# Kernel optimization log

Hardware: AMD Instinct MI355X
Metric: run time of the kernel (lower is better)

Reference implementation:

```python
import jax, jax.numpy as jnp
import numpy as np

N = 500_000   # total points
B = 8         # scenes / segments
C = 64        # embedding_dim (= internal_dim, downsample_rate=1)
H = 8         # num_heads


def setup_inputs() -> dict:
    key = jax.random.key(0)
    ks = jax.random.split(key, 12)
    s = 1.0 / np.sqrt(C)
    q = jax.random.normal(ks[0], (N, C), jnp.float32)
    k = jax.random.normal(ks[1], (B, C), jnp.float32)
    v = jax.random.normal(ks[2], (B, C), jnp.float32)
    batch = jnp.sort(jax.random.randint(ks[3], (N,), 0, B)).astype(jnp.int64)
    Wq = jax.random.normal(ks[4], (C, C), jnp.float32) * s
    bq = jnp.zeros((C,), jnp.float32)
    Wk = jax.random.normal(ks[5], (C, C), jnp.float32) * s
    bk = jnp.zeros((C,), jnp.float32)
    Wv = jax.random.normal(ks[6], (C, C), jnp.float32) * s
    bv = jnp.zeros((C,), jnp.float32)
    Wo = jax.random.normal(ks[7], (C, C), jnp.float32) * s
    bo = jnp.zeros((C,), jnp.float32)
    return dict(q=q, k=k, v=v, Wq=Wq, bq=bq, Wk=Wk, bk=bk, Wv=Wv, bv=bv,
                Wo=Wo, bo=bo, batch=batch)


def reference(q, k, v, Wq, bq, Wk, bk, Wv, bv, Wo, bo, batch):
    # Linear projections (nn.Linear applies x @ W.T + b)
    qp = q @ Wq.T + bq            # [N, C]
    kp = k @ Wk.T + bk            # [B, C]
    vp = v @ Wv.T + bv            # [B, C]
    n, c = qp.shape
    d = c // H                    # c_per_head
    nb = kp.shape[0]
    qh = qp.reshape(n, H, d)
    kh = kp.reshape(nb, H, d)[batch]   # gather per point -> [N, H, d]
    vh = vp.reshape(nb, H, d)[batch]   # [N, H, d]
    # elementwise scores, scaled
    attn = qh * kh * (1.0 / np.sqrt(d))  # [N, H, d]
    # segment softmax over the point dim within each batch segment
    m = jax.ops.segment_max(attn, batch, num_segments=nb)   # [B, H, d]
    e = jnp.exp(attn - m[batch])
    z = jax.ops.segment_sum(e, batch, num_segments=nb)      # [B, H, d]
    a = e / z[batch]
    out = (a * vh).reshape(n, c)
    return out @ Wo.T + bo
```

## Files before the change

kernel.cpp:

```cpp
#include <hip/hip_runtime.h>
#include <math.h>

#define NPTS 500000
#define SCALE 0.35355339059327373f
#define NTILES 7813
#define TPB 4
#define GRID ((NTILES + TPB - 1) / TPB)

#define QT_IDX(k, p) ((((k) >> 2) * 276) + (((k) & 3) * 68) + (p))
#define QT_SIZE 4416


__global__ void prep_kernel(const float* __restrict__ kin, const float* __restrict__ vin,
                            const float* __restrict__ Wq, const float* __restrict__ Wk,
                            const float* __restrict__ bk, const float* __restrict__ Wv,
                            const float* __restrict__ bv, const float* __restrict__ Wo,
                            float* __restrict__ ws) {
    const int gid = blockIdx.x * 256 + threadIdx.x;
    float* WqT = ws;
    float* WoT = ws + 4096;
    float* khs = ws + 8192;
    float* vh  = ws + 8704;
    double* zg = (double*)(ws + 9216);
    for (int idx = gid; idx < 4096; idx += 8 * 256) {
        int a = idx >> 6, b = idx & 63;
        WqT[idx] = Wq[b * 64 + a];
        WoT[idx] = Wo[b * 64 + a];
    }
    for (int idx = gid; idx < 512; idx += 8 * 256) {
        int b = idx >> 6, c = idx & 63;
        float dk = 0.f, dv = 0.f;
        #pragma unroll 8
        for (int j = 0; j < 64; ++j) {
            dk = fmaf(kin[b * 64 + j], Wk[c * 64 + j], dk);
            dv = fmaf(vin[b * 64 + j], Wv[c * 64 + j], dv);
        }
        khs[idx] = (dk + bk[c]) * SCALE;
        vh[idx]  = dv + bv[c];
        zg[idx]  = 0.0;
    }
}

__global__ __launch_bounds__(256, 4) void passA_kernel(const float* __restrict__ q,
                                                       const int* __restrict__ batch,
                                                       const float* __restrict__ bq,
                                                       float* __restrict__ ws,
                                                       float* __restrict__ e_out) {
    __shared__ __align__(16) float qT[QT_SIZE];
    __shared__ __align__(16) float wq[4096];
    __shared__ __align__(16) float khs_l[512];
    __shared__ __align__(16) float bq_l[64];
    __shared__ int bs[64];
    __shared__ __align__(16) float zred[4 * 64];

    const float* WqT   = ws;
    const float* khs_g = ws + 8192;
    double* zg = (double*)(ws + 9216);

    const int tid = threadIdx.x;
    const int tx = tid & 15, ty = tid >> 4;

    for (int idx = tid; idx < 1024; idx += 256) ((float4*)wq)[idx] = ((const float4*)WqT)[idx];
    for (int idx = tid; idx < 128; idx += 256) ((float4*)khs_l)[idx] = ((const float4*)khs_g)[idx];
    if (tid < 64) bq_l[tid] = bq[tid];

    float zacc[4] = {0.f, 0.f, 0.f, 0.f};
    int cur_b = -1;

    auto flushz = [&](int b) {
        if (b < 0) return;
        float v0 = zacc[0], v1 = zacc[1], v2 = zacc[2], v3 = zacc[3];
        v0 += __shfl_xor(v0, 16); v0 += __shfl_xor(v0, 32);
        v1 += __shfl_xor(v1, 16); v1 += __shfl_xor(v1, 32);
        v2 += __shfl_xor(v2, 16); v2 += __shfl_xor(v2, 32);
        v3 += __shfl_xor(v3, 16); v3 += __shfl_xor(v3, 32);
        __syncthreads();
        if ((tid & 48) == 0) {
            int wv = tid >> 6;
            *(float4*)&zred[wv * 64 + 4 * tx] = make_float4(v0, v1, v2, v3);
        }
        __syncthreads();
        if (tid < 64) {
            float s = zred[tid] + zred[64 + tid] + zred[128 + tid] + zred[192 + tid];
            unsafeAtomicAdd(&zg[b * 64 + tid], (double)s);
        }
        zacc[0] = zacc[1] = zacc[2] = zacc[3] = 0.f;
    };

    const int t0 = blockIdx.x * TPB;
    const int t1 = (t0 + TPB < NTILES) ? (t0 + TPB) : NTILES;
    __syncthreads();

    float bqa[4];
    { float4 b4 = *(const float4*)&bq_l[4 * tx];
      bqa[0] = b4.x; bqa[1] = b4.y; bqa[2] = b4.z; bqa[3] = b4.w; }

    for (int t = t0; t < t1; ++t) {
        const int p0g = t * 64;
        #pragma unroll
        for (int r = 0; r < 4; ++r) {
            int p = ty + r * 16;
            int gp = p0g + p;
            float4 val = make_float4(0.f, 0.f, 0.f, 0.f);
            if (gp < NPTS) val = ((const float4*)q)[gp * 16 + tx];
            qT[QT_IDX(4 * tx + 0, p)] = val.x;
            qT[QT_IDX(4 * tx + 1, p)] = val.y;
            qT[QT_IDX(4 * tx + 2, p)] = val.z;
            qT[QT_IDX(4 * tx + 3, p)] = val.w;
        }
        if (tid < 64) {
            int gp = p0g + tid;
            bs[tid] = batch[gp < NPTS ? gp : (NPTS - 1)];
        }
        __syncthreads();
        const int b_lo = bs[0], b_hi = bs[63];
        const bool uni = (b_lo == b_hi);
        if (uni) {
            if (cur_b != b_lo) { flushz(cur_b); cur_b = b_lo; }
        } else {
            flushz(cur_b); cur_b = -1;
        }

        float acc[4][4] = {};
        #pragma unroll 4
        for (int kg = 0; kg < 16; ++kg) {
            #pragma unroll
            for (int kj = 0; kj < 4; ++kj) {
                float4 a4 = *(const float4*)&qT[kg * 276 + kj * 68 + 4 * ty];
                float4 w4 = *(const float4*)&wq[(kg * 4 + kj) * 64 + 4 * tx];
                float av[4] = {a4.x, a4.y, a4.z, a4.w};
                float wv[4] = {w4.x, w4.y, w4.z, w4.w};
                #pragma unroll
                for (int i = 0; i < 4; ++i)
                    #pragma unroll
                    for (int j = 0; j < 4; ++j)
                        acc[i][j] = fmaf(av[i], wv[j], acc[i][j]);
            }
        }

        float ev[4][4];
        #pragma unroll
        for (int i = 0; i < 4; ++i) {
            int pl = 4 * ty + i, gp = p0g + pl;
            int bi = bs[pl];
            float4 k4 = *(const float4*)&khs_l[bi * 64 + 4 * tx];
            float kh[4] = {k4.x, k4.y, k4.z, k4.w};
            bool valid = (gp < NPTS);
            #pragma unroll
            for (int j = 0; j < 4; ++j)
                ev[i][j] = valid ? __expf((acc[i][j] + bqa[j]) * kh[j]) : 0.f;
            if (valid)
                ((float4*)e_out)[gp * 16 + tx] = make_float4(ev[i][0], ev[i][1], ev[i][2], ev[i][3]);
        }

        if (uni) {
            #pragma unroll
            for (int j = 0; j < 4; ++j)
                zacc[j] += (ev[0][j] + ev[1][j]) + (ev[2][j] + ev[3][j]);
        } else {
            #pragma unroll
            for (int i = 0; i < 4; ++i) {
                int pl = 4 * ty + i, gp = p0g + pl;
                int bi = bs[pl];
                if (gp < NPTS) {
                    #pragma unroll
                    for (int j = 0; j < 4; ++j)
                        unsafeAtomicAdd(&zg[bi * 64 + 4 * tx + j], (double)ev[i][j]);
                }
            }
        }
        __syncthreads();
    }
    flushz(cur_b);
}

__global__ __launch_bounds__(256, 4) void passB_kernel(const int* __restrict__ batch,
                                                       const float* __restrict__ bo,
                                                       const float* __restrict__ ws,
                                                       float* __restrict__ out) {
    __shared__ __align__(16) float tT[QT_SIZE];
    __shared__ __align__(16) float wo[4096];
    __shared__ __align__(16) float w_l[512];
    __shared__ __align__(16) float bo_l[64];

    const float* WoT  = ws + 4096;
    const float* vh_g = ws + 8704;
    const double* zg  = (const double*)(ws + 9216);

    const int tid = threadIdx.x;
    const int tx = tid & 15, ty = tid >> 4;

    for (int idx = tid; idx < 1024; idx += 256) ((float4*)wo)[idx] = ((const float4*)WoT)[idx];
    for (int idx = tid; idx < 512; idx += 256)
        w_l[idx] = (float)((double)vh_g[idx] / zg[idx]);
    if (tid < 64) bo_l[tid] = bo[tid];

    const int t0 = blockIdx.x * TPB;
    const int t1 = (t0 + TPB < NTILES) ? (t0 + TPB) : NTILES;
    __syncthreads();

    float boa[4];
    { float4 b4 = *(const float4*)&bo_l[4 * tx];
      boa[0] = b4.x; boa[1] = b4.y; boa[2] = b4.z; boa[3] = b4.w; }

    for (int t = t0; t < t1; ++t) {
        const int p0g = t * 64;
        #pragma unroll
        for (int r = 0; r < 4; ++r) {
            int p = ty + r * 16;
            int gp = p0g + p;
            float4 ev = make_float4(0.f, 0.f, 0.f, 0.f);
            int bi = 0;
            if (gp < NPTS) { ev = ((const float4*)out)[gp * 16 + tx]; bi = batch[gp]; }
            float4 wv = *(const float4*)&w_l[bi * 64 + 4 * tx];
            tT[QT_IDX(4 * tx + 0, p)] = ev.x * wv.x;
            tT[QT_IDX(4 * tx + 1, p)] = ev.y * wv.y;
            tT[QT_IDX(4 * tx + 2, p)] = ev.z * wv.z;
            tT[QT_IDX(4 * tx + 3, p)] = ev.w * wv.w;
        }
        __syncthreads();

        float acc[4][4] = {};
        #pragma unroll 4
        for (int cg = 0; cg < 16; ++cg) {
            #pragma unroll
            for (int cj = 0; cj < 4; ++cj) {
                float4 a4 = *(const float4*)&tT[cg * 276 + cj * 68 + 4 * ty];
                float4 w4 = *(const float4*)&wo[(cg * 4 + cj) * 64 + 4 * tx];
                float av[4] = {a4.x, a4.y, a4.z, a4.w};
                float wv[4] = {w4.x, w4.y, w4.z, w4.w};
                #pragma unroll
                for (int i = 0; i < 4; ++i)
                    #pragma unroll
                    for (int j = 0; j < 4; ++j)
                        acc[i][j] = fmaf(av[i], wv[j], acc[i][j]);
            }
        }

        #pragma unroll
        for (int i = 0; i < 4; ++i) {
            int gp = p0g + 4 * ty + i;
            if (gp < NPTS) {
                float4 o = make_float4(acc[i][0] + boa[0], acc[i][1] + boa[1],
                                       acc[i][2] + boa[2], acc[i][3] + boa[3]);
                ((float4*)out)[gp * 16 + tx] = o;
            }
        }
        __syncthreads();
    }
}

extern "C" void kernel_launch(void* const* d_in, const int* in_sizes, int n_in,
                              void* d_out, int out_size, void* d_ws, size_t ws_size,
                              hipStream_t stream) {
    const float* q   = (const float*)d_in[0];
    const float* k   = (const float*)d_in[1];
    const float* v   = (const float*)d_in[2];
    const float* Wq  = (const float*)d_in[3];
    const float* bq  = (const float*)d_in[4];
    const float* Wk  = (const float*)d_in[5];
    const float* bk  = (const float*)d_in[6];
    const float* Wv  = (const float*)d_in[7];
    const float* bv  = (const float*)d_in[8];
    const float* Wo  = (const float*)d_in[9];
    const float* bo  = (const float*)d_in[10];
    const int*  batch = (const int*)d_in[11];
    float* out = (float*)d_out;
    float* ws  = (float*)d_ws;

    prep_kernel<<<8, 256, 0, stream>>>(k, v, Wq, Wk, bk, Wv, bv, Wo, ws);
    passA_kernel<<<GRID, 256, 0, stream>>>(q, batch, bq, ws, out);
    passB_kernel<<<GRID, 256, 0, stream>>>(batch, bo, ws, out);
}
```

Before: 346.2 us.

## Keep weight slices in registers and split K across lanes with LDS reduction

Both GEMM passes now hold a 16x4 slice of the weight matrix in registers per lane, split the 64-wide reduction across four lane groups, and combine partial sums through a padded LDS scratch within each wavefront. The q/out tiles are loaded into LDS with coalesced float4 copies and no transpose, which removes the shared weight copy and the transposed tile. In pass B the per-segment softmax normalizer is folded into the register weights when a tile belongs to a single segment. This trades the LDS weight traffic for more registers per lane and an extra intra-wave reduction step, and relies on wavefront-synchronous LDS access with only a compiler barrier between the write and the read.

```diff
diff --git a/kernel.cpp b/kernel.cpp
--- a/kernel.cpp
+++ b/kernel.cpp
@@ -6,10 +6,18 @@
 #define NTILES 7813
 #define TPB 4
 #define GRID ((NTILES + TPB - 1) / TPB)
-
-#define QT_IDX(k, p) ((((k) >> 2) * 276) + (((k) & 3) * 68) + (p))
-#define QT_SIZE 4416
-
+#define Q4TOT 8000000
+
+
+#define FMA4(A, S, W) do { A.x = fmaf(S, W.x, A.x); A.y = fmaf(S, W.y, A.y); \
+                           A.z = fmaf(S, W.z, A.z); A.w = fmaf(S, W.w, A.w); } while (0)
+
+#define FMABLK(A, a0, a1, a2, a3) do { \
+    FMA4(A, a0.x, wr[0]);  FMA4(A, a0.y, wr[1]);  FMA4(A, a0.z, wr[2]);  FMA4(A, a0.w, wr[3]);  \
+    FMA4(A, a1.x, wr[4]);  FMA4(A, a1.y, wr[5]);  FMA4(A, a1.z, wr[6]);  FMA4(A, a1.w, wr[7]);  \
+    FMA4(A, a2.x, wr[8]);  FMA4(A, a2.y, wr[9]);  FMA4(A, a2.z, wr[10]); FMA4(A, a2.w, wr[11]); \
+    FMA4(A, a3.x, wr[12]); FMA4(A, a3.y, wr[13]); FMA4(A, a3.z, wr[14]); FMA4(A, a3.w, wr[15]); \
+} while (0)
 
 __global__ void prep_kernel(const float* __restrict__ kin, const float* __restrict__ vin,
                             const float* __restrict__ Wq, const float* __restrict__ Wk,
@@ -46,126 +54,127 @@
                                                        const float* __restrict__ bq,
                                                        float* __restrict__ ws,
                                                        float* __restrict__ e_out) {
-    __shared__ __align__(16) float qT[QT_SIZE];
-    __shared__ __align__(16) float wq[4096];
-    __shared__ __align__(16) float khs_l[512];
-    __shared__ __align__(16) float bq_l[64];
-    __shared__ int bs[64];
-    __shared__ __align__(16) float zred[4 * 64];
+    __shared__ __align__(16) float qtile[4096];
+    __shared__ __align__(16) float4 red[4 * 272];
+    __shared__ __align__(16) float zred[256];
 
     const float* WqT   = ws;
     const float* khs_g = ws + 8192;
     double* zg = (double*)(ws + 9216);
 
-    const int tid = threadIdx.x;
-    const int tx = tid & 15, ty = tid >> 4;
-
-    for (int idx = tid; idx < 1024; idx += 256) ((float4*)wq)[idx] = ((const float4*)WqT)[idx];
-    for (int idx = tid; idx < 128; idx += 256) ((float4*)khs_l)[idx] = ((const float4*)khs_g)[idx];
-    if (tid < 64) bq_l[tid] = bq[tid];
-
-    float zacc[4] = {0.f, 0.f, 0.f, 0.f};
+    const int tid  = threadIdx.x;
+    const int wid  = tid >> 6;
+    const int lane = tid & 63;
+    const int tx   = lane & 15;
+    const int ky   = lane >> 4;
+
+    float4* redw = red + wid * 272;
+
+    float4 wr[16];
+    #pragma unroll
+    for (int kk = 0; kk < 16; ++kk)
+        wr[kk] = *(const float4*)&WqT[(ky * 16 + kk) * 64 + 4 * tx];
+
+    const float4 bq4 = ((const float4*)bq)[tx];
+
+    float4 zacc = make_float4(0.f, 0.f, 0.f, 0.f);
     int cur_b = -1;
 
     auto flushz = [&](int b) {
         if (b < 0) return;
-        float v0 = zacc[0], v1 = zacc[1], v2 = zacc[2], v3 = zacc[3];
-        v0 += __shfl_xor(v0, 16); v0 += __shfl_xor(v0, 32);
-        v1 += __shfl_xor(v1, 16); v1 += __shfl_xor(v1, 32);
-        v2 += __shfl_xor(v2, 16); v2 += __shfl_xor(v2, 32);
-        v3 += __shfl_xor(v3, 16); v3 += __shfl_xor(v3, 32);
-        __syncthreads();
-        if ((tid & 48) == 0) {
-            int wv = tid >> 6;
-            *(float4*)&zred[wv * 64 + 4 * tx] = make_float4(v0, v1, v2, v3);
-        }
+        float4 v = zacc;
+        v.x += __shfl_xor(v.x, 16); v.y += __shfl_xor(v.y, 16);
+        v.z += __shfl_xor(v.z, 16); v.w += __shfl_xor(v.w, 16);
+        v.x += __shfl_xor(v.x, 32); v.y += __shfl_xor(v.y, 32);
+        v.z += __shfl_xor(v.z, 32); v.w += __shfl_xor(v.w, 32);
+        __syncthreads();
+        if (ky == 0) *(float4*)&zred[wid * 64 + 4 * tx] = v;
         __syncthreads();
         if (tid < 64) {
             float s = zred[tid] + zred[64 + tid] + zred[128 + tid] + zred[192 + tid];
             unsafeAtomicAdd(&zg[b * 64 + tid], (double)s);
         }
-        zacc[0] = zacc[1] = zacc[2] = zacc[3] = 0.f;
+        zacc = make_float4(0.f, 0.f, 0.f, 0.f);
     };
 
     const int t0 = blockIdx.x * TPB;
     const int t1 = (t0 + TPB < NTILES) ? (t0 + TPB) : NTILES;
-    __syncthreads();
-
-    float bqa[4];
-    { float4 b4 = *(const float4*)&bq_l[4 * tx];
-      bqa[0] = b4.x; bqa[1] = b4.y; bqa[2] = b4.z; bqa[3] = b4.w; }
 
     for (int t = t0; t < t1; ++t) {
         const int p0g = t * 64;
+
         #pragma unroll
-        for (int r = 0; r < 4; ++r) {
-            int p = ty + r * 16;
-            int gp = p0g + p;
-            float4 val = make_float4(0.f, 0.f, 0.f, 0.f);
-            if (gp < NPTS) val = ((const float4*)q)[gp * 16 + tx];
-            qT[QT_IDX(4 * tx + 0, p)] = val.x;
-            qT[QT_IDX(4 * tx + 1, p)] = val.y;
-            qT[QT_IDX(4 * tx + 2, p)] = val.z;
-            qT[QT_IDX(4 * tx + 3, p)] = val.w;
-        }
-        if (tid < 64) {
-            int gp = p0g + tid;
-            bs[tid] = batch[gp < NPTS ? gp : (NPTS - 1)];
-        }
-        __syncthreads();
-        const int b_lo = bs[0], b_hi = bs[63];
+        for (int i = 0; i < 4; ++i) {
+            const int g4 = t * 1024 + i * 256 + tid;
+            float4 v = make_float4(0.f, 0.f, 0.f, 0.f);
+            if (g4 < Q4TOT) v = ((const float4*)q)[g4];
+            ((float4*)qtile)[i * 256 + tid] = v;
+        }
+        const int b_lo = batch[p0g];
+        const int b_hi = batch[(p0g + 63 < NPTS) ? (p0g + 63) : (NPTS - 1)];
         const bool uni = (b_lo == b_hi);
+        __syncthreads();
+
         if (uni) {
             if (cur_b != b_lo) { flushz(cur_b); cur_b = b_lo; }
         } else {
-            flushz(cur_b); cur_b = -1;
-        }
-
-        float acc[4][4] = {};
-        #pragma unroll 4
-        for (int kg = 0; kg < 16; ++kg) {
-            #pragma unroll
-            for (int kj = 0; kj < 4; ++kj) {
-                float4 a4 = *(const float4*)&qT[kg * 276 + kj * 68 + 4 * ty];
-                float4 w4 = *(const float4*)&wq[(kg * 4 + kj) * 64 + 4 * tx];
-                float av[4] = {a4.x, a4.y, a4.z, a4.w};
-                float wv[4] = {w4.x, w4.y, w4.z, w4.w};
-                #pragma unroll
-                for (int i = 0; i < 4; ++i)
-                    #pragma unroll
-                    for (int j = 0; j < 4; ++j)
-                        acc[i][j] = fmaf(av[i], wv[j], acc[i][j]);
-            }
-        }
-
-        float ev[4][4];
-        #pragma unroll
-        for (int i = 0; i < 4; ++i) {
-            int pl = 4 * ty + i, gp = p0g + pl;
-            int bi = bs[pl];
-            float4 k4 = *(const float4*)&khs_l[bi * 64 + 4 * tx];
-            float kh[4] = {k4.x, k4.y, k4.z, k4.w};
-            bool valid = (gp < NPTS);
-            #pragma unroll
-            for (int j = 0; j < 4; ++j)
-                ev[i][j] = valid ? __expf((acc[i][j] + bqa[j]) * kh[j]) : 0.f;
-            if (valid)
-                ((float4*)e_out)[gp * 16 + tx] = make_float4(ev[i][0], ev[i][1], ev[i][2], ev[i][3]);
-        }
-
-        if (uni) {
-            #pragma unroll
-            for (int j = 0; j < 4; ++j)
-                zacc[j] += (ev[0][j] + ev[1][j]) + (ev[2][j] + ev[3][j]);
-        } else {
+            flushz(cur_b);
+            cur_b = -1;
+        }
+
+        const float4 kh4 = *(const float4*)&khs_g[b_lo * 64 + 4 * tx];
+
+        for (int pass = 0; pass < 4; ++pass) {
+            const int pl0 = wid * 16 + pass * 4;
+            float4 acc[4];
+            #pragma unroll
+            for (int i = 0; i < 4; ++i) acc[i] = make_float4(0.f, 0.f, 0.f, 0.f);
+
             #pragma unroll
             for (int i = 0; i < 4; ++i) {
-                int pl = 4 * ty + i, gp = p0g + pl;
-                int bi = bs[pl];
-                if (gp < NPTS) {
-                    #pragma unroll
-                    for (int j = 0; j < 4; ++j)
-                        unsafeAtomicAdd(&zg[bi * 64 + 4 * tx + j], (double)ev[i][j]);
+                const float4* r = (const float4*)(qtile + (pl0 + i) * 64 + ky * 16);
+                const float4 a0 = r[0], a1 = r[1], a2 = r[2], a3 = r[3];
+                FMABLK(acc[i], a0, a1, a2, a3);
+            }
+
+            #pragma unroll
+            for (int i = 0; i < 4; ++i) redw[(i * 4 + ky) * 17 + tx] = acc[i];
+            asm volatile("" ::: "memory");
+            const float4 s0 = redw[(ky * 4 + 0) * 17 + tx];
+            const float4 s1 = redw[(ky * 4 + 1) * 17 + tx];
+            const float4 s2 = redw[(ky * 4 + 2) * 17 + tx];
+            const float4 s3 = redw[(ky * 4 + 3) * 17 + tx];
+            float4 s;
+            s.x = (s0.x + s1.x) + (s2.x + s3.x);
+            s.y = (s0.y + s1.y) + (s2.y + s3.y);
+            s.z = (s0.z + s1.z) + (s2.z + s3.z);
+            s.w = (s0.w + s1.w) + (s2.w + s3.w);
+
+            const int gp = p0g + pl0 + ky;
+            const bool valid = (gp < NPTS);
+
+            if (uni) {
+                float4 e4;
+                e4.x = valid ? __expf((s.x + bq4.x) * kh4.x) : 0.f;
+                e4.y = valid ? __expf((s.y + bq4.y) * kh4.y) : 0.f;
+                e4.z = valid ? __expf((s.z + bq4.z) * kh4.z) : 0.f;
+                e4.w = valid ? __expf((s.w + bq4.w) * kh4.w) : 0.f;
+                if (valid) ((float4*)e_out)[gp * 16 + tx] = e4;
+                zacc.x += e4.x; zacc.y += e4.y; zacc.z += e4.z; zacc.w += e4.w;
+            } else {
+                const int bpt = batch[valid ? gp : (NPTS - 1)];
+                const float4 kh = *(const float4*)&khs_g[bpt * 64 + 4 * tx];
+                float4 e4;
+                e4.x = __expf((s.x + bq4.x) * kh.x);
+                e4.y = __expf((s.y + bq4.y) * kh.y);
+                e4.z = __expf((s.z + bq4.z) * kh.z);
+                e4.w = __expf((s.w + bq4.w) * kh.w);
+                if (valid) {
+                    ((float4*)e_out)[gp * 16 + tx] = e4;
+                    unsafeAtomicAdd(&zg[bpt * 64 + 4 * tx + 0], (double)e4.x);
+                    unsafeAtomicAdd(&zg[bpt * 64 + 4 * tx + 1], (double)e4.y);
+                    unsafeAtomicAdd(&zg[bpt * 64 + 4 * tx + 2], (double)e4.z);
+                    unsafeAtomicAdd(&zg[bpt * 64 + 4 * tx + 3], (double)e4.w);
                 }
             }
         }
@@ -178,71 +187,106 @@
                                                        const float* __restrict__ bo,
                                                        const float* __restrict__ ws,
                                                        float* __restrict__ out) {
-    __shared__ __align__(16) float tT[QT_SIZE];
-    __shared__ __align__(16) float wo[4096];
+    __shared__ __align__(16) float ttile[4096];
+    __shared__ __align__(16) float4 red[4 * 272];
     __shared__ __align__(16) float w_l[512];
-    __shared__ __align__(16) float bo_l[64];
 
     const float* WoT  = ws + 4096;
     const float* vh_g = ws + 8704;
     const double* zg  = (const double*)(ws + 9216);
 
-    const int tid = threadIdx.x;
-    const int tx = tid & 15, ty = tid >> 4;
-
-    for (int idx = tid; idx < 1024; idx += 256) ((float4*)wo)[idx] = ((const float4*)WoT)[idx];
+    const int tid  = threadIdx.x;
+    const int wid  = tid >> 6;
+    const int lane = tid & 63;
+    const int tx   = lane & 15;
+    const int ky   = lane >> 4;
+
+    float4* redw = red + wid * 272;
+
     for (int idx = tid; idx < 512; idx += 256)
         w_l[idx] = (float)((double)vh_g[idx] / zg[idx]);
-    if (tid < 64) bo_l[tid] = bo[tid];
+
+    const float4 bo4 = ((const float4*)bo)[tx];
+
+    float4 wr[16];
+    int wb = -2;
 
     const int t0 = blockIdx.x * TPB;
     const int t1 = (t0 + TPB < NTILES) ? (t0 + TPB) : NTILES;
+
     __syncthreads();
-
-    float boa[4];
-    { float4 b4 = *(const float4*)&bo_l[4 * tx];
-      boa[0] = b4.x; boa[1] = b4.y; boa[2] = b4.z; boa[3] = b4.w; }
 
     for (int t = t0; t < t1; ++t) {
         const int p0g = t * 64;
-        #pragma unroll
-        for (int r = 0; r < 4; ++r) {
-            int p = ty + r * 16;
-            int gp = p0g + p;
-            float4 ev = make_float4(0.f, 0.f, 0.f, 0.f);
-            int bi = 0;
-            if (gp < NPTS) { ev = ((const float4*)out)[gp * 16 + tx]; bi = batch[gp]; }
-            float4 wv = *(const float4*)&w_l[bi * 64 + 4 * tx];
-            tT[QT_IDX(4 * tx + 0, p)] = ev.x * wv.x;
-            tT[QT_IDX(4 * tx + 1, p)] = ev.y * wv.y;
-            tT[QT_IDX(4 * tx + 2, p)] = ev.z * wv.z;
-            tT[QT_IDX(4 * tx + 3, p)] = ev.w * wv.w;
-        }
-        __syncthreads();
-
-        float acc[4][4] = {};
-        #pragma unroll 4
-        for (int cg = 0; cg < 16; ++cg) {
-            #pragma unroll
-            for (int cj = 0; cj < 4; ++cj) {
-                float4 a4 = *(const float4*)&tT[cg * 276 + cj * 68 + 4 * ty];
-                float4 w4 = *(const float4*)&wo[(cg * 4 + cj) * 64 + 4 * tx];
-                float av[4] = {a4.x, a4.y, a4.z, a4.w};
-                float wv[4] = {w4.x, w4.y, w4.z, w4.w};
-                #pragma unroll
-                for (int i = 0; i < 4; ++i)
-                    #pragma unroll
-                    for (int j = 0; j < 4; ++j)
-                        acc[i][j] = fmaf(av[i], wv[j], acc[i][j]);
-            }
-        }
 
         #pragma unroll
         for (int i = 0; i < 4; ++i) {
-            int gp = p0g + 4 * ty + i;
+            const int g4 = t * 1024 + i * 256 + tid;
+            float4 v = make_float4(0.f, 0.f, 0.f, 0.f);
+            if (g4 < Q4TOT) v = ((const float4*)out)[g4];
+            ((float4*)ttile)[i * 256 + tid] = v;
+        }
+        const int b_lo = batch[p0g];
+        const int b_hi = batch[(p0g + 63 < NPTS) ? (p0g + 63) : (NPTS - 1)];
+        const bool uni = (b_lo == b_hi);
+        __syncthreads();
+
+        if (uni) {
+            if (wb != b_lo) {
+                #pragma unroll
+                for (int kk = 0; kk < 16; ++kk) {
+                    const float m = w_l[b_lo * 64 + ky * 16 + kk];
+                    float4 wv = *(const float4*)&WoT[(ky * 16 + kk) * 64 + 4 * tx];
+                    wv.x *= m; wv.y *= m; wv.z *= m; wv.w *= m;
+                    wr[kk] = wv;
+                }
+                wb = b_lo;
+            }
+        } else if (wb != -1) {
+            #pragma unroll
+            for (int kk = 0; kk < 16; ++kk)
+                wr[kk] = *(const float4*)&WoT[(ky * 16 + kk) * 64 + 4 * tx];
+            wb = -1;
+        }
+
+        for (int pass = 0; pass < 4; ++pass) {
+            const int pl0 = wid * 16 + pass * 4;
+            float4 acc[4];
+            #pragma unroll
+            for (int i = 0; i < 4; ++i) acc[i] = make_float4(0.f, 0.f, 0.f, 0.f);
+
+            #pragma unroll
+            for (int i = 0; i < 4; ++i) {
+                const float4* r = (const float4*)(ttile + (pl0 + i) * 64 + ky * 16);
+                float4 a0 = r[0], a1 = r[1], a2 = r[2], a3 = r[3];
+                if (!uni) {
+                    const int gpi = p0g + pl0 + i;
+                    const int bp = batch[(gpi < NPTS) ? gpi : (NPTS - 1)];
+                    const float4* wrow = (const float4*)&w_l[bp * 64 + ky * 16];
+                    const float4 m0 = wrow[0], m1 = wrow[1], m2 = wrow[2], m3 = wrow[3];
+                    a0.x *= m0.x; a0.y *= m0.y; a0.z *= m0.z; a0.w *= m0.w;
+                    a1.x *= m1.x; a1.y *= m1.y; a1.z *= m1.z; a1.w *= m1.w;
+                    a2.x *= m2.x; a2.y *= m2.y; a2.z *= m2.z; a2.w *= m2.w;
+                    a3.x *= m3.x; a3.y *= m3.y; a3.z *= m3.z; a3.w *= m3.w;
+                }
+                FMABLK(acc[i], a0, a1, a2, a3);
+            }
+
+            #pragma unroll
+            for (int i = 0; i < 4; ++i) redw[(i * 4 + ky) * 17 + tx] = acc[i];
+            asm volatile("" ::: "memory");
+            const float4 s0 = redw[(ky * 4 + 0) * 17 + tx];
+            const float4 s1 = redw[(ky * 4 + 1) * 17 + tx];
+            const float4 s2 = redw[(ky * 4 + 2) * 17 + tx];
+            const float4 s3 = redw[(ky * 4 + 3) * 17 + tx];
+
+            const int gp = p0g + pl0 + ky;
             if (gp < NPTS) {
-                float4 o = make_float4(acc[i][0] + boa[0], acc[i][1] + boa[1],
-                                       acc[i][2] + boa[2], acc[i][3] + boa[3]);
+                float4 o;
+                o.x = ((s0.x + s1.x) + (s2.x + s3.x)) + bo4.x;
+                o.y = ((s0.y + s1.y) + (s2.y + s3.y)) + bo4.y;
+                o.z = ((s0.z + s1.z) + (s2.z + s3.z)) + bo4.z;
+                o.w = ((s0.w + s1.w) + (s2.w + s3.w)) + bo4.w;
                 ((float4*)out)[gp * 16 + tx] = o;
             }
         }
```

After: 943.3 us. +172.5%, slower.

## Enlarge point tiles to 128 with 4x8 register blocking in both GEMM passes

Applied to the files above, without the earlier changes.

Both passes now process 128-point tiles with each thread computing a 4x8 output block (two float4 column groups), which roughly halves LDS traffic per FMA. Global loads of q/e are made fully linear float4 reads. The per-tile batch id buffer is replaced by reading the tile's first and last batch ids from global memory, with per-point lookups only on segment-boundary tiles. Bias moves to registers. The cost is more registers and LDS per block, so occupancy drops (launch bounds lowered to 3), and there are fewer tiles per block.

```diff
diff --git a/kernel.cpp b/kernel.cpp
--- a/kernel.cpp
+++ b/kernel.cpp
@@ -3,12 +3,13 @@
 
 #define NPTS 500000
 #define SCALE 0.35355339059327373f
-#define NTILES 7813
-#define TPB 4
-#define GRID ((NTILES + TPB - 1) / TPB)
-
-#define QT_IDX(k, p) ((((k) >> 2) * 276) + (((k) & 3) * 68) + (p))
-#define QT_SIZE 4416
+#define NT128 3907
+#define TPB 2
+#define GRID ((NT128 + TPB - 1) / TPB)
+#define Q4TOT 8000000
+
+#define QTIDX(k, p) ((((k) >> 2) * 532) + (((k) & 3) * 132) + (p))
+#define QT_SZ 8512
 
 
 __global__ void prep_kernel(const float* __restrict__ kin, const float* __restrict__ vin,
@@ -41,131 +42,158 @@
     }
 }
 
-__global__ __launch_bounds__(256, 4) void passA_kernel(const float* __restrict__ q,
+
+__global__ __launch_bounds__(256, 3) void passA_kernel(const float* __restrict__ q,
                                                        const int* __restrict__ batch,
                                                        const float* __restrict__ bq,
                                                        float* __restrict__ ws,
                                                        float* __restrict__ e_out) {
-    __shared__ __align__(16) float qT[QT_SIZE];
+    __shared__ __align__(16) float qT[QT_SZ];
     __shared__ __align__(16) float wq[4096];
     __shared__ __align__(16) float khs_l[512];
-    __shared__ __align__(16) float bq_l[64];
-    __shared__ int bs[64];
-    __shared__ __align__(16) float zred[4 * 64];
+    __shared__ __align__(16) float zred[256];
 
     const float* WqT   = ws;
     const float* khs_g = ws + 8192;
     double* zg = (double*)(ws + 9216);
 
-    const int tid = threadIdx.x;
-    const int tx = tid & 15, ty = tid >> 4;
+    const int tid  = threadIdx.x;
+    const int wid  = tid >> 6;
+    const int lane = tid & 63;
+    const int cc   = tid & 7;
+    const int ty   = tid >> 3;
 
     for (int idx = tid; idx < 1024; idx += 256) ((float4*)wq)[idx] = ((const float4*)WqT)[idx];
     for (int idx = tid; idx < 128; idx += 256) ((float4*)khs_l)[idx] = ((const float4*)khs_g)[idx];
-    if (tid < 64) bq_l[tid] = bq[tid];
-
-    float zacc[4] = {0.f, 0.f, 0.f, 0.f};
+
+    float bqlo[4], bqhi[4];
+    { float4 b4 = ((const float4*)bq)[cc];
+      bqlo[0] = b4.x; bqlo[1] = b4.y; bqlo[2] = b4.z; bqlo[3] = b4.w;
+      b4 = ((const float4*)bq)[8 + cc];
+      bqhi[0] = b4.x; bqhi[1] = b4.y; bqhi[2] = b4.z; bqhi[3] = b4.w; }
+
+    float zacc[8] = {};
     int cur_b = -1;
 
     auto flushz = [&](int b) {
         if (b < 0) return;
-        float v0 = zacc[0], v1 = zacc[1], v2 = zacc[2], v3 = zacc[3];
-        v0 += __shfl_xor(v0, 16); v0 += __shfl_xor(v0, 32);
-        v1 += __shfl_xor(v1, 16); v1 += __shfl_xor(v1, 32);
-        v2 += __shfl_xor(v2, 16); v2 += __shfl_xor(v2, 32);
-        v3 += __shfl_xor(v3, 16); v3 += __shfl_xor(v3, 32);
-        __syncthreads();
-        if ((tid & 48) == 0) {
-            int wv = tid >> 6;
-            *(float4*)&zred[wv * 64 + 4 * tx] = make_float4(v0, v1, v2, v3);
+        #pragma unroll
+        for (int j = 0; j < 8; ++j) {
+            zacc[j] += __shfl_xor(zacc[j], 8);
+            zacc[j] += __shfl_xor(zacc[j], 16);
+            zacc[j] += __shfl_xor(zacc[j], 32);
+        }
+        __syncthreads();
+        if ((lane >> 3) == 0) {
+            *(float4*)&zred[wid * 64 + 4 * cc]      = make_float4(zacc[0], zacc[1], zacc[2], zacc[3]);
+            *(float4*)&zred[wid * 64 + 32 + 4 * cc] = make_float4(zacc[4], zacc[5], zacc[6], zacc[7]);
         }
         __syncthreads();
         if (tid < 64) {
             float s = zred[tid] + zred[64 + tid] + zred[128 + tid] + zred[192 + tid];
             unsafeAtomicAdd(&zg[b * 64 + tid], (double)s);
         }
-        zacc[0] = zacc[1] = zacc[2] = zacc[3] = 0.f;
+        #pragma unroll
+        for (int j = 0; j < 8; ++j) zacc[j] = 0.f;
     };
 
     const int t0 = blockIdx.x * TPB;
-    const int t1 = (t0 + TPB < NTILES) ? (t0 + TPB) : NTILES;
+    const int t1 = (t0 + TPB < NT128) ? (t0 + TPB) : NT128;
     __syncthreads();
 
-    float bqa[4];
-    { float4 b4 = *(const float4*)&bq_l[4 * tx];
-      bqa[0] = b4.x; bqa[1] = b4.y; bqa[2] = b4.z; bqa[3] = b4.w; }
-
     for (int t = t0; t < t1; ++t) {
-        const int p0g = t * 64;
-        #pragma unroll
-        for (int r = 0; r < 4; ++r) {
-            int p = ty + r * 16;
-            int gp = p0g + p;
-            float4 val = make_float4(0.f, 0.f, 0.f, 0.f);
-            if (gp < NPTS) val = ((const float4*)q)[gp * 16 + tx];
-            qT[QT_IDX(4 * tx + 0, p)] = val.x;
-            qT[QT_IDX(4 * tx + 1, p)] = val.y;
-            qT[QT_IDX(4 * tx + 2, p)] = val.z;
-            qT[QT_IDX(4 * tx + 3, p)] = val.w;
-        }
-        if (tid < 64) {
-            int gp = p0g + tid;
-            bs[tid] = batch[gp < NPTS ? gp : (NPTS - 1)];
-        }
-        __syncthreads();
-        const int b_lo = bs[0], b_hi = bs[63];
+        const int p0g = t * 128;
+
+        #pragma unroll
+        for (int i = 0; i < 8; ++i) {
+            const int g4 = t * 2048 + i * 256 + tid;
+            float4 v = make_float4(0.f, 0.f, 0.f, 0.f);
+            if (g4 < Q4TOT) v = ((const float4*)q)[g4];
+            const int pl = i * 16 + (tid >> 4);
+            const int kc = tid & 15;
+            qT[QTIDX(4 * kc + 0, pl)] = v.x;
+            qT[QTIDX(4 * kc + 1, pl)] = v.y;
+            qT[QTIDX(4 * kc + 2, pl)] = v.z;
+            qT[QTIDX(4 * kc + 3, pl)] = v.w;
+        }
+        const int b_lo = batch[p0g];
+        const int b_hi = batch[(p0g + 127 < NPTS) ? (p0g + 127) : (NPTS - 1)];
         const bool uni = (b_lo == b_hi);
+        __syncthreads();
+
         if (uni) {
             if (cur_b != b_lo) { flushz(cur_b); cur_b = b_lo; }
         } else {
-            flushz(cur_b); cur_b = -1;
-        }
-
-        float acc[4][4] = {};
+            flushz(cur_b);
+            cur_b = -1;
+        }
+
+        float acc[4][8] = {};
         #pragma unroll 4
-        for (int kg = 0; kg < 16; ++kg) {
+        for (int kc = 0; kc < 16; ++kc) {
             #pragma unroll
-            for (int kj = 0; kj < 4; ++kj) {
-                float4 a4 = *(const float4*)&qT[kg * 276 + kj * 68 + 4 * ty];
-                float4 w4 = *(const float4*)&wq[(kg * 4 + kj) * 64 + 4 * tx];
-                float av[4] = {a4.x, a4.y, a4.z, a4.w};
-                float wv[4] = {w4.x, w4.y, w4.z, w4.w};
+            for (int j = 0; j < 4; ++j) {
+                const float4 a4  = *(const float4*)&qT[kc * 532 + j * 132 + 4 * ty];
+                const float4 wlo = *(const float4*)&wq[(kc * 4 + j) * 64 + 4 * cc];
+                const float4 whi = *(const float4*)&wq[(kc * 4 + j) * 64 + 32 + 4 * cc];
+                const float av[4] = {a4.x, a4.y, a4.z, a4.w};
+                const float wl[4] = {wlo.x, wlo.y, wlo.z, wlo.w};
+                const float wh[4] = {whi.x, whi.y, whi.z, whi.w};
                 #pragma unroll
-                for (int i = 0; i < 4; ++i)
-                    #pragma unroll
-                    for (int j = 0; j < 4; ++j)
-                        acc[i][j] = fmaf(av[i], wv[j], acc[i][j]);
-            }
-        }
-
-        float ev[4][4];
-        #pragma unroll
-        for (int i = 0; i < 4; ++i) {
-            int pl = 4 * ty + i, gp = p0g + pl;
-            int bi = bs[pl];
-            float4 k4 = *(const float4*)&khs_l[bi * 64 + 4 * tx];
-            float kh[4] = {k4.x, k4.y, k4.z, k4.w};
-            bool valid = (gp < NPTS);
+                for (int i = 0; i < 4; ++i) {
+                    #pragma unroll
+                    for (int m = 0; m < 4; ++m) {
+                        acc[i][m]     = fmaf(av[i], wl[m], acc[i][m]);
+                        acc[i][4 + m] = fmaf(av[i], wh[m], acc[i][4 + m]);
+                    }
+                }
+            }
+        }
+
+        if (uni) {
+            const float4 klo = *(const float4*)&khs_l[b_lo * 64 + 4 * cc];
+            const float4 khi = *(const float4*)&khs_l[b_lo * 64 + 32 + 4 * cc];
+            const float kl[4] = {klo.x, klo.y, klo.z, klo.w};
+            const float kh[4] = {khi.x, khi.y, khi.z, khi.w};
             #pragma unroll
-            for (int j = 0; j < 4; ++j)
-                ev[i][j] = valid ? __expf((acc[i][j] + bqa[j]) * kh[j]) : 0.f;
-            if (valid)
-                ((float4*)e_out)[gp * 16 + tx] = make_float4(ev[i][0], ev[i][1], ev[i][2], ev[i][3]);
-        }
-
-        if (uni) {
-            #pragma unroll
-            for (int j = 0; j < 4; ++j)
-                zacc[j] += (ev[0][j] + ev[1][j]) + (ev[2][j] + ev[3][j]);
+            for (int i = 0; i < 4; ++i) {
+                const int gp = p0g + 4 * ty + i;
+                if (gp < NPTS) {
+                    float e0[4], e1[4];
+                    #pragma unroll
+                    for (int m = 0; m < 4; ++m) {
+                        e0[m] = __expf((acc[i][m] + bqlo[m]) * kl[m]);
+                        e1[m] = __expf((acc[i][4 + m] + bqhi[m]) * kh[m]);
+                    }
+                    ((float4*)e_out)[gp * 16 + cc]     = make_float4(e0[0], e0[1], e0[2], e0[3]);
+                    ((float4*)e_out)[gp * 16 + 8 + cc] = make_float4(e1[0], e1[1], e1[2], e1[3]);
+                    #pragma unroll
+                    for (int m = 0; m < 4; ++m) { zacc[m] += e0[m]; zacc[4 + m] += e1[m]; }
+                }
+            }
         } else {
             #pragma unroll
             for (int i = 0; i < 4; ++i) {
-                int pl = 4 * ty + i, gp = p0g + pl;
-                int bi = bs[pl];
+                const int gp = p0g + 4 * ty + i;
                 if (gp < NPTS) {
-                    #pragma unroll
-                    for (int j = 0; j < 4; ++j)
-                        unsafeAtomicAdd(&zg[bi * 64 + 4 * tx + j], (double)ev[i][j]);
+                    const int bi = batch[gp];
+                    const float4 klo = *(const float4*)&khs_l[bi * 64 + 4 * cc];
+                    const float4 khi = *(const float4*)&khs_l[bi * 64 + 32 + 4 * cc];
+                    const float kl[4] = {klo.x, klo.y, klo.z, klo.w};
+                    const float kh[4] = {khi.x, khi.y, khi.z, khi.w};
+                    float e0[4], e1[4];
+                    #pragma unroll
+                    for (int m = 0; m < 4; ++m) {
+                        e0[m] = __expf((acc[i][m] + bqlo[m]) * kl[m]);
+                        e1[m] = __expf((acc[i][4 + m] + bqhi[m]) * kh[m]);
+                    }
+                    ((float4*)e_out)[gp * 16 + cc]     = make_float4(e0[0], e0[1], e0[2], e0[3]);
+                    ((float4*)e_out)[gp * 16 + 8 + cc] = make_float4(e1[0], e1[1], e1[2], e1[3]);
+                    #pragma unroll
+                    for (int m = 0; m < 4; ++m) {
+                        unsafeAtomicAdd(&zg[bi * 64 + 4 * cc + m], (double)e0[m]);
+                        unsafeAtomicAdd(&zg[bi * 64 + 32 + 4 * cc + m], (double)e1[m]);
+                    }
                 }
             }
         }
@@ -174,76 +202,94 @@
     flushz(cur_b);
 }
 
-__global__ __launch_bounds__(256, 4) void passB_kernel(const int* __restrict__ batch,
+__global__ __launch_bounds__(256, 3) void passB_kernel(const int* __restrict__ batch,
                                                        const float* __restrict__ bo,
                                                        const float* __restrict__ ws,
                                                        float* __restrict__ out) {
-    __shared__ __align__(16) float tT[QT_SIZE];
+    __shared__ __align__(16) float tT[QT_SZ];
     __shared__ __align__(16) float wo[4096];
     __shared__ __align__(16) float w_l[512];
-    __shared__ __align__(16) float bo_l[64];
 
     const float* WoT  = ws + 4096;
     const float* vh_g = ws + 8704;
     const double* zg  = (const double*)(ws + 9216);
 
     const int tid = threadIdx.x;
-    const int tx = tid & 15, ty = tid >> 4;
+    const int cc  = tid & 7;
+    const int ty  = tid >> 3;
 
     for (int idx = tid; idx < 1024; idx += 256) ((float4*)wo)[idx] = ((const float4*)WoT)[idx];
     for (int idx = tid; idx < 512; idx += 256)
         w_l[idx] = (float)((double)vh_g[idx] / zg[idx]);
-    if (tid < 64) bo_l[tid] = bo[tid];
+
+    float bolo[4], bohi[4];
+    { float4 b4 = ((const float4*)bo)[cc];
+      bolo[0] = b4.x; bolo[1] = b4.y; bolo[2] = b4.z; bolo[3] = b4.w;
+      b4 = ((const float4*)bo)[8 + cc];
+      bohi[0] = b4.x; bohi[1] = b4.y; bohi[2] = b4.z; bohi[3] = b4.w; }
 
     const int t0 = blockIdx.x * TPB;
-    const int t1 = (t0 + TPB < NTILES) ? (t0 + TPB) : NTILES;
+    const int t1 = (t0 + TPB < NT128) ? (t0 + TPB) : NT128;
     __syncthreads();
 
-    float boa[4];
-    { float4 b4 = *(const float4*)&bo_l[4 * tx];
-      boa[0] = b4.x; boa[1] = b4.y; boa[2] = b4.z; boa[3] = b4.w; }
-
     for (int t = t0; t < t1; ++t) {
-        const int p0g = t * 64;
-        #pragma unroll
-        for (int r = 0; r < 4; ++r) {
-            int p = ty + r * 16;
-            int gp = p0g + p;
-            float4 ev = make_float4(0.f, 0.f, 0.f, 0.f);
-            int bi = 0;
-            if (gp < NPTS) { ev = ((const float4*)out)[gp * 16 + tx]; bi = batch[gp]; }
-            float4 wv = *(const float4*)&w_l[bi * 64 + 4 * tx];
-            tT[QT_IDX(4 * tx + 0, p)] = ev.x * wv.x;
-            tT[QT_IDX(4 * tx + 1, p)] = ev.y * wv.y;
-            tT[QT_IDX(4 * tx + 2, p)] = ev.z * wv.z;
-            tT[QT_IDX(4 * tx + 3, p)] = ev.w * wv.w;
-        }
-        __syncthreads();
-
-        float acc[4][4] = {};
+        const int p0g = t * 128;
+        const int b_lo = batch[p0g];
+        const int b_hi = batch[(p0g + 127 < NPTS) ? (p0g + 127) : (NPTS - 1)];
+        const bool uni = (b_lo == b_hi);
+
+        #pragma unroll
+        for (int i = 0; i < 8; ++i) {
+            const int g4 = t * 2048 + i * 256 + tid;
+            float4 v = make_float4(0.f, 0.f, 0.f, 0.f);
+            if (g4 < Q4TOT) v = ((const float4*)out)[g4];
+            const int pl = i * 16 + (tid >> 4);
+            const int kc = tid & 15;
+            int bi = b_lo;
+            if (!uni) {
+                const int gp = p0g + pl;
+                bi = batch[(gp < NPTS) ? gp : (NPTS - 1)];
+            }
+            const float4 wv = *(const float4*)&w_l[bi * 64 + 4 * kc];
+            tT[QTIDX(4 * kc + 0, pl)] = v.x * wv.x;
+            tT[QTIDX(4 * kc + 1, pl)] = v.y * wv.y;
+            tT[QTIDX(4 * kc + 2, pl)] = v.z * wv.z;
+            tT[QTIDX(4 * kc + 3, pl)] = v.w * wv.w;
+        }
+        __syncthreads();
+
+        float acc[4][8] = {};
         #pragma unroll 4
-        for (int cg = 0; cg < 16; ++cg) {
+        for (int kc = 0; kc < 16; ++kc) {
             #pragma unroll
-            for (int cj = 0; cj < 4; ++cj) {
-                float4 a4 = *(const float4*)&tT[cg * 276 + cj * 68 + 4 * ty];
-                float4 w4 = *(const float4*)&wo[(cg * 4 + cj) * 64 + 4 * tx];
-                float av[4] = {a4.x, a4.y, a4.z, a4.w};
-                float wv[4] = {w4.x, w4.y, w4.z, w4.w};
+            for (int j = 0; j < 4; ++j) {
+                const float4 a4  = *(const float4*)&tT[kc * 532 + j * 132 + 4 * ty];
+                const float4 wlo = *(const float4*)&wo[(kc * 4 + j) * 64 + 4 * cc];
+                const float4 whi = *(const float4*)&wo[(kc * 4 + j) * 64 + 32 + 4 * cc];
+                const float av[4] = {a4.x, a4.y, a4.z, a4.w};
+                const float wl[4] = {wlo.x, wlo.y, wlo.z, wlo.w};
+                const float wh[4] = {whi.x, whi.y, whi.z, whi.w};
                 #pragma unroll
-                for (int i = 0; i < 4; ++i)
-                    #pragma unroll
-                    for (int j = 0; j < 4; ++j)
-                        acc[i][j] = fmaf(av[i], wv[j], acc[i][j]);
+                for (int i = 0; i < 4; ++i) {
+                    #pragma unroll
+                    for (int m = 0; m < 4; ++m) {
+                        acc[i][m]     = fmaf(av[i], wl[m], acc[i][m]);
+                        acc[i][4 + m] = fmaf(av[i], wh[m], acc[i][4 + m]);
+                    }
+                }
             }
         }
 
         #pragma unroll
         for (int i = 0; i < 4; ++i) {
-            int gp = p0g + 4 * ty + i;
+            const int gp = p0g + 4 * ty + i;
             if (gp < NPTS) {
-                float4 o = make_float4(acc[i][0] + boa[0], acc[i][1] + boa[1],
-                                       acc[i][2] + boa[2], acc[i][3] + boa[3]);
-                ((float4*)out)[gp * 16 + tx] = o;
+                ((float4*)out)[gp * 16 + cc] =
+                    make_float4(acc[i][0] + bolo[0], acc[i][1] + bolo[1],
+                                acc[i][2] + bolo[2], acc[i][3] + bolo[3]);
+                ((float4*)out)[gp * 16 + 8 + cc] =
+                    make_float4(acc[i][4] + bohi[0], acc[i][5] + bohi[1],
+                                acc[i][6] + bohi[2], acc[i][7] + bohi[3]);
             }
         }
         __syncthreads();
```

Measured after the change: 349.6 us. About the same (+1.0%).
